# Performance work log

Hardware: AMD Instinct MI355X
Metric: run time of the kernel (lower is better)

Reference implementation:

```python
import jax, jax.numpy as jnp
import numpy as np

E = 200_000   # number of edges (messages)
T = 500_000   # number of triplets
H = 128       # hidden_channels
B = 8         # num_bilinear
R = 6         # num_radial
S = 7         # num_spherical


def setup_inputs() -> dict:
    key = jax.random.key(0)
    ks = jax.random.split(key, 18)
    w = 0.05  # small init scale for numerical stability
    return {
        "x":   jax.random.normal(ks[0], (E, H), dtype=jnp.float32),
        "rbf": jax.random.normal(ks[1], (E, R), dtype=jnp.float32),
        "sbf": jax.random.normal(ks[2], (T, S * R), dtype=jnp.float32),
        "idx_kj": jax.random.randint(ks[3], (T,), 0, E),
        "idx_ji": jax.random.randint(ks[4], (T,), 0, E),
        # parameters (stored as [in, out] so we apply x @ w)
        "lin_rbf_w": jax.random.normal(ks[5], (R, H), dtype=jnp.float32) * w,
        "lin_sbf_w": jax.random.normal(ks[6], (S * R, B), dtype=jnp.float32) * w,
        "lin_kj_w": jax.random.normal(ks[7], (H, H), dtype=jnp.float32) * w,
        "lin_kj_b": jnp.zeros((H,), dtype=jnp.float32),
        "lin_ji_w": jax.random.normal(ks[8], (H, H), dtype=jnp.float32) * w,
        "lin_ji_b": jnp.zeros((H,), dtype=jnp.float32),
        "W": jax.random.normal(ks[9], (H, B, H), dtype=jnp.float32) * (2.0 / H),
        "before_w": jax.random.normal(ks[10], (1, 2, H, H), dtype=jnp.float32) * w,
        "before_b": jnp.zeros((1, 2, H), dtype=jnp.float32),
        "lin_w": jax.random.normal(ks[11], (H, H), dtype=jnp.float32) * w,
        "lin_b": jnp.zeros((H,), dtype=jnp.float32),
        "after_w": jax.random.normal(ks[12], (2, 2, H, H), dtype=jnp.float32) * w,
        "after_b": jnp.zeros((2, 2, H), dtype=jnp.float32),
    }


def _residual(h, w2, b2):
    # DimeNet ResidualLayer: h + act(lin2(act(lin1(h))))
    return h + jax.nn.silu(jax.nn.silu(h @ w2[0] + b2[0]) @ w2[1] + b2[1])


def reference(x, rbf, sbf, idx_kj, idx_ji,
              lin_rbf_w, lin_sbf_w, lin_kj_w, lin_kj_b,
              lin_ji_w, lin_ji_b, W,
              before_w, before_b, lin_w, lin_b, after_w, after_b):
    act = jax.nn.silu
    rbf_p = rbf @ lin_rbf_w                     # [E, H]
    sbf_p = sbf @ lin_sbf_w                     # [T, B]
    x_ji = act(x @ lin_ji_w + lin_ji_b)         # [E, H]
    x_kj = act(x @ lin_kj_w + lin_kj_b) * rbf_p # [E, H]
    g = x_kj[idx_kj]                            # gather -> [T, H]
    # bilinear: 'wj,wl,ijl->wi' with i,l=hidden, j=bilinear
    m = jnp.einsum('wj,wl,ijl->wi', sbf_p, g, W)  # [T, H]
    agg = jax.ops.segment_sum(m, idx_ji, num_segments=x.shape[0])  # [E, H]
    h = x_ji + agg
    for i in range(before_w.shape[0]):
        h = _residual(h, before_w[i], before_b[i])
    h = act(h @ lin_w + lin_b) + x
    for i in range(after_w.shape[0]):
        h = _residual(h, after_w[i], after_b[i])
    return h
```

## Files before the change

kernel.cpp:

```cpp
#include <hip/hip_runtime.h>

#define E_N 200000
#define T_N 500000

typedef __attribute__((ext_vector_type(8))) short bf16x8;
typedef __attribute__((ext_vector_type(4))) float f32x4;
typedef unsigned short u16;
typedef unsigned int u32;

#define SWZ(b) ((b) ^ ((((b) >> 8) & 7) << 4))

#define SYNC_DRAIN() do { asm volatile("s_waitcnt vmcnt(0)" ::: "memory"); __syncthreads(); } while (0)

__device__ __forceinline__ u16 f2bf(float f){
  u32 u = __float_as_uint(f);
  return (u16)((u + 0x7fffu + ((u >> 16) & 1u)) >> 16);
}
__device__ __forceinline__ float silu_f(float v){
  return __fdividef(v, 1.f + __expf(-v));
}
__device__ __forceinline__ void gl_lds16(const void* g, void* l){
  __builtin_amdgcn_global_load_lds((const __attribute__((address_space(1))) u32*)g,
                                   (__attribute__((address_space(3))) u32*)l, 16, 0, 0);
}
__device__ __forceinline__ bf16x8 scale8(uint4 g, float s){
  union { bf16x8 v; u32 u[4]; } aa;
  u32 gu[4] = { g.x, g.y, g.z, g.w };
  #pragma unroll
  for (int q = 0; q < 4; q++){
    float lo = __uint_as_float(gu[q] << 16) * s;
    float hi = __uint_as_float(gu[q] & 0xffff0000u) * s;
    asm("v_cvt_pk_bf16_f32 %0, %1, %2" : "=v"(aa.u[q]) : "v"(lo), "v"(hi));
  }
  return aa.v;
}

__device__ __forceinline__ void gemm_tile(const char* ldsA, const char* ldsB,
                                          int wv, int lane, f32x4 acc[8]){
  const int arow = wv*16 + (lane & 15);
  const int kof = (lane >> 4) << 3;
  #pragma unroll
  for (int kc = 0; kc < 4; kc++){
    const int kb = (kc*32 + kof)*2;
    bf16x8 a = *(const bf16x8*)(ldsA + SWZ(arow*256 + kb));
    #pragma unroll
    for (int n = 0; n < 8; n++){
      bf16x8 b = *(const bf16x8*)(ldsB + SWZ((n*16 + (lane & 15))*256 + kb));
      acc[n] = __builtin_amdgcn_mfma_f32_16x16x32_bf16(a, b, acc[n], 0, 0, 0);
    }
  }
}

__global__ __launch_bounds__(256) void k_cvt_W(const float* __restrict__ W, u16* __restrict__ out){
  int i = blockIdx.x*256 + threadIdx.x;
  out[i] = f2bf(W[i]);
}

__global__ __launch_bounds__(256) void k_cvt_T(const float* __restrict__ jiw, const float* __restrict__ kjw,
                                               const float* __restrict__ bw, const float* __restrict__ lw,
                                               const float* __restrict__ aw, u16* __restrict__ out){
  int i = blockIdx.x*256 + threadIdx.x;
  int m = i >> 14, o = i & 16383;
  int n = o >> 7, k = o & 127;
  const float* src;
  switch (m){
    case 0: src = jiw; break;
    case 1: src = kjw; break;
    case 2: src = bw; break;
    case 3: src = bw + 16384; break;
    case 4: src = lw; break;
    default: src = aw + (m - 5)*16384; break;
  }
  out[i] = f2bf(src[k*128 + n]);
}

__global__ __launch_bounds__(256) void k_edge(const float* __restrict__ x, const float* __restrict__ rbf,
    const float* __restrict__ rbfw, const u16* __restrict__ wji, const u16* __restrict__ wkj,
    const float* __restrict__ bji, const float* __restrict__ bkj,
    float* __restrict__ out, u16* __restrict__ xkj)
{
  __shared__ __align__(16) char ldsA[16384];
  __shared__ __align__(16) char ldsB[32768];
  __shared__ float lrbf[64*6];
  __shared__ float lrbfw[6*128];
  __shared__ float lbj[128];
  __shared__ float lbk[128];
  const int tid = threadIdx.x;
  const int e0 = blockIdx.x * 64;

  #pragma unroll
  for (int it = 0; it < 4; it++){
    int i = it*256 + tid;
    int row = i >> 4, c8 = (i & 15) << 3;
    const float4* s = (const float4*)(x + (e0 + row)*128 + c8);
    float4 v0 = s[0], v1 = s[1];
    union { u16 us[8]; uint4 q; } u;
    u.us[0]=f2bf(v0.x); u.us[1]=f2bf(v0.y); u.us[2]=f2bf(v0.z); u.us[3]=f2bf(v0.w);
    u.us[4]=f2bf(v1.x); u.us[5]=f2bf(v1.y); u.us[6]=f2bf(v1.z); u.us[7]=f2bf(v1.w);
    *(uint4*)(ldsA + SWZ(row*256 + c8*2)) = u.q;
  }
  #pragma unroll
  for (int it = 0; it < 8; it++){
    int p = (it*256 + tid)*16;
    int pb = __builtin_amdgcn_readfirstlane(p);
    int n = p >> 8, o = p & 255;
    gl_lds16((const char*)wji + n*256 + (o ^ ((n & 7) << 4)), ldsB + pb);
  }
  for (int i = tid; i < 384; i += 256) lrbf[i] = rbf[e0*6 + i];
  for (int i = tid; i < 768; i += 256) lrbfw[i] = rbfw[i];
  if (tid < 128){ lbj[tid] = bji[tid]; lbk[tid] = bkj[tid]; }
  SYNC_DRAIN();

  const int wv = tid >> 6, lane = tid & 63;
  const int colb = lane & 15, rgrp = (lane >> 4) << 2;
  f32x4 acc[8];
  #pragma unroll
  for (int n = 0; n < 8; n++)
    #pragma unroll
    for (int r = 0; r < 4; r++) acc[n][r] = 0.f;
  gemm_tile(ldsA, ldsB, wv, lane, acc);
  #pragma unroll
  for (int n = 0; n < 8; n++){
    int col = n*16 + colb;
    float b = lbj[col];
    #pragma unroll
    for (int r = 0; r < 4; r++){
      int row = e0 + wv*16 + rgrp + r;
      out[row*128 + col] = silu_f(acc[n][r] + b);
    }
  }
  __syncthreads();
  #pragma unroll
  for (int it = 0; it < 8; it++){
    int p = (it*256 + tid)*16;
    int pb = __builtin_amdgcn_readfirstlane(p);
    int n = p >> 8, o = p & 255;
    gl_lds16((const char*)wkj + n*256 + (o ^ ((n & 7) << 4)), ldsB + pb);
  }
  SYNC_DRAIN();
  #pragma unroll
  for (int n = 0; n < 8; n++)
    #pragma unroll
    for (int r = 0; r < 4; r++) acc[n][r] = 0.f;
  gemm_tile(ldsA, ldsB, wv, lane, acc);

  float rb[4][6];
  #pragma unroll
  for (int r = 0; r < 4; r++)
    #pragma unroll
    for (int c = 0; c < 6; c++) rb[r][c] = lrbf[(wv*16 + rgrp + r)*6 + c];
  #pragma unroll
  for (int n = 0; n < 8; n++){
    int col = n*16 + colb;
    float b = lbk[col];
    float wc[6];
    #pragma unroll
    for (int c = 0; c < 6; c++) wc[c] = lrbfw[c*128 + col];
    #pragma unroll
    for (int r = 0; r < 4; r++){
      float rp = 0.f;
      #pragma unroll
      for (int c = 0; c < 6; c++) rp += rb[r][c]*wc[c];
      int row = e0 + wv*16 + rgrp + r;
      xkj[row*128 + col] = f2bf(silu_f(acc[n][r] + b) * rp);
    }
  }
}

__device__ __forceinline__ void stage_Wslice(const u16* __restrict__ Wbf, int j, char* dst, int tid){
  #pragma unroll
  for (int it = 0; it < 4; it++){
    int p = (it*512 + tid)*16;
    int pb = __builtin_amdgcn_readfirstlane(p);
    int n = p >> 8, o = p & 255;
    gl_lds16((const char*)Wbf + n*2048 + j*256 + (o ^ ((n & 7) << 4)), dst + pb);
  }
}

__global__ __launch_bounds__(512, 4) void k_trip(
    const u16* __restrict__ xkj, const float* __restrict__ sbf, const float* __restrict__ sbfw,
    const int* __restrict__ idx_kj, const int* __restrict__ idx_ji, const u16* __restrict__ Wbf,
    float* __restrict__ out)
{
  __shared__ __align__(16) char ldsW[2][32768];
  __shared__ float lss[256*8];
  __shared__ float lsw[336];
  __shared__ int lji[256];
  __shared__ int lkj[256];
  const int tid = threadIdx.x;
  const int t0 = blockIdx.x * 256;

  {
    float* scr = (float*)ldsW;
    for (int i = tid; i < 256*42; i += 512){
      int gi = t0*42 + i;
      scr[i] = (gi < T_N*42) ? sbf[gi] : 0.f;
    }
  }
  for (int i = tid; i < 336; i += 512) lsw[i] = sbfw[i];
  if (tid < 256){
    int w = t0 + tid;
    lji[tid] = (w < T_N) ? idx_ji[w] : -1;
    lkj[tid] = (w < T_N) ? idx_kj[w] : 0;
  }
  __syncthreads();

  const int wv = tid >> 6, lane = tid & 63;
  const int r15 = lane & 15, q = lane >> 4;

  uint4 graw[8];
  #pragma unroll
  for (int rt = 0; rt < 2; rt++){
    int row = lkj[wv*32 + rt*16 + r15];
    const char* src = (const char*)xkj + (long)row*256 + q*16;
    #pragma unroll
    for (int kc = 0; kc < 4; kc++)
      graw[rt*4 + kc] = *(const uint4*)(src + kc*64);
  }
  if (tid < 256){
    const float* scr = (const float*)ldsW;
    float a[8];
    #pragma unroll
    for (int k = 0; k < 8; k++) a[k] = 0.f;
    for (int c = 0; c < 42; c++){
      float v = scr[tid*42 + c];
      #pragma unroll
      for (int k = 0; k < 8; k++) a[k] += v * lsw[c*8 + k];
    }
    #pragma unroll
    for (int k = 0; k < 8; k++) lss[tid*8 + k] = a[k];
  }
  __syncthreads();
  stage_Wslice(Wbf, 0, ldsW[0], tid);
  SYNC_DRAIN();

  f32x4 acc0[8], acc1[8];
  #pragma unroll
  for (int n = 0; n < 8; n++)
    #pragma unroll
    for (int r = 0; r < 4; r++){ acc0[n][r] = 0.f; acc1[n][r] = 0.f; }

  const int swz_lane = (r15 & 7) << 4;
  for (int j = 0; j < 8; j++){
    const char* bp = ldsW[j & 1];
    if (j < 7) stage_Wslice(Wbf, j + 1, ldsW[(j + 1) & 1], tid);
    const float s0 = lss[(wv*32 + r15)*8 + j];
    const float s1 = lss[(wv*32 + 16 + r15)*8 + j];
    #pragma unroll
    for (int kc = 0; kc < 4; kc++){
      const int ab = (r15*256 + q*16 + kc*64) ^ swz_lane;
      bf16x8 aa0 = scale8(graw[kc], s0);
      bf16x8 aa1 = scale8(graw[4 + kc], s1);
      #pragma unroll
      for (int n = 0; n < 8; n++){
        bf16x8 b = *(const bf16x8*)(bp + n*4096 + ab);
        acc0[n] = __builtin_amdgcn_mfma_f32_16x16x32_bf16(aa0, b, acc0[n], 0, 0, 0);
        acc1[n] = __builtin_amdgcn_mfma_f32_16x16x32_bf16(aa1, b, acc1[n], 0, 0, 0);
      }
    }
    SYNC_DRAIN();
  }

  const int rgrp = q << 2;
  #pragma unroll
  for (int n = 0; n < 8; n++){
    const int col = n*16 + r15;
    #pragma unroll
    for (int r = 0; r < 4; r++){
      int e0i = lji[wv*32 + rgrp + r];
      if (e0i >= 0) unsafeAtomicAdd(out + e0i*128 + col, acc0[n][r]);
      int e1i = lji[wv*32 + 16 + rgrp + r];
      if (e1i >= 0) unsafeAtomicAdd(out + e1i*128 + col, acc1[n][r]);
    }
  }
}

__global__ __launch_bounds__(256) void k_epi(
    const float* __restrict__ x, float* __restrict__ hio, const u16* __restrict__ wm,
    const float* __restrict__ bb2, const float* __restrict__ linb, const float* __restrict__ ab2)
{
  __shared__ __align__(16) char ldsA[16384];
  __shared__ __align__(16) char ldsB[32768];
  __shared__ float lbias[7][128];
  const int tid = threadIdx.x;
  const int e0 = blockIdx.x * 64;
  if (tid < 128){
    lbias[0][tid] = bb2[tid];
    lbias[1][tid] = bb2[128 + tid];
    lbias[2][tid] = linb[tid];
    lbias[3][tid] = ab2[tid];
    lbias[4][tid] = ab2[128 + tid];
    lbias[5][tid] = ab2[256 + tid];
    lbias[6][tid] = ab2[384 + tid];
  }
  const int wv = tid >> 6, lane = tid & 63;
  const int colb = lane & 15, rgrp = (lane >> 4) << 2;
  float h[8][4], t[8][4];
  f32x4 acc[8];
  #pragma unroll
  for (int n = 0; n < 8; n++)
    #pragma unroll
    for (int r = 0; r < 4; r++)
      h[n][r] = hio[(e0 + wv*16 + rgrp + r)*128 + n*16 + colb];

#define STAGE_B(mi) { \
  _Pragma("unroll") \
  for (int it = 0; it < 8; it++){ \
    int p = (it*256 + tid)*16; \
    int pb = __builtin_amdgcn_readfirstlane(p); \
    int nn = p >> 8, o = p & 255; \
    gl_lds16((const char*)wm + (mi)*32768 + nn*256 + (o ^ ((nn & 7) << 4)), ldsB + pb); \
  } }
#define WRITE_A(v) { \
  _Pragma("unroll") \
  for (int n = 0; n < 8; n++){ \
    _Pragma("unroll") \
    for (int r = 0; r < 4; r++){ \
      int rowl = wv*16 + rgrp + r; \
      *(u16*)(ldsA + SWZ(rowl*256 + (n*16 + colb)*2)) = f2bf(v[n][r]); \
    } } }
#define RUN_GEMM() { \
  _Pragma("unroll") \
  for (int n = 0; n < 8; n++){ \
    _Pragma("unroll") \
    for (int r = 0; r < 4; r++) acc[n][r] = 0.f; } \
  gemm_tile(ldsA, ldsB, wv, lane, acc); }

  STAGE_B(0); WRITE_A(h); SYNC_DRAIN(); RUN_GEMM();
  #pragma unroll
  for (int n = 0; n < 8; n++){ float b = lbias[0][n*16 + colb];
    #pragma unroll
    for (int r = 0; r < 4; r++) t[n][r] = silu_f(acc[n][r] + b); }
  __syncthreads(); STAGE_B(1); WRITE_A(t); SYNC_DRAIN(); RUN_GEMM();
  #pragma unroll
  for (int n = 0; n < 8; n++){ float b = lbias[1][n*16 + colb];
    #pragma unroll
    for (int r = 0; r < 4; r++) h[n][r] += silu_f(acc[n][r] + b); }
  __syncthreads(); STAGE_B(2); WRITE_A(h); SYNC_DRAIN(); RUN_GEMM();
  #pragma unroll
  for (int n = 0; n < 8; n++){ float b = lbias[2][n*16 + colb];
    #pragma unroll
    for (int r = 0; r < 4; r++)
      h[n][r] = silu_f(acc[n][r] + b) + x[(e0 + wv*16 + rgrp + r)*128 + n*16 + colb]; }
  __syncthreads(); STAGE_B(3); WRITE_A(h); SYNC_DRAIN(); RUN_GEMM();
  #pragma unroll
  for (int n = 0; n < 8; n++){ float b = lbias[3][n*16 + colb];
    #pragma unroll
    for (int r = 0; r < 4; r++) t[n][r] = silu_f(acc[n][r] + b); }
  __syncthreads(); STAGE_B(4); WRITE_A(t); SYNC_DRAIN(); RUN_GEMM();
  #pragma unroll
  for (int n = 0; n < 8; n++){ float b = lbias[4][n*16 + colb];
    #pragma unroll
    for (int r = 0; r < 4; r++) h[n][r] += silu_f(acc[n][r] + b); }
  __syncthreads(); STAGE_B(5); WRITE_A(h); SYNC_DRAIN(); RUN_GEMM();
  #pragma unroll
  for (int n = 0; n < 8; n++){ float b = lbias[5][n*16 + colb];
    #pragma unroll
    for (int r = 0; r < 4; r++) t[n][r] = silu_f(acc[n][r] + b); }
  __syncthreads(); STAGE_B(6); WRITE_A(t); SYNC_DRAIN(); RUN_GEMM();
  #pragma unroll
  for (int n = 0; n < 8; n++){ float b = lbias[6][n*16 + colb];
    #pragma unroll
    for (int r = 0; r < 4; r++) h[n][r] += silu_f(acc[n][r] + b); }

  #pragma unroll
  for (int n = 0; n < 8; n++)
    #pragma unroll
    for (int r = 0; r < 4; r++)
      hio[(e0 + wv*16 + rgrp + r)*128 + n*16 + colb] = h[n][r];
#undef STAGE_B
#undef WRITE_A
#undef RUN_GEMM
}

extern "C" void kernel_launch(void* const* d_in, const int* in_sizes, int n_in,
                              void* d_out, int out_size, void* d_ws, size_t ws_size,
                              hipStream_t stream)
{
  const float* x    = (const float*)d_in[0];
  const float* rbf  = (const float*)d_in[1];
  const float* sbf  = (const float*)d_in[2];
  const int* idx_kj = (const int*)d_in[3];
  const int* idx_ji = (const int*)d_in[4];
  const float* rbfw = (const float*)d_in[5];
  const float* sbfw = (const float*)d_in[6];
  const float* kjw  = (const float*)d_in[7];
  const float* kjb  = (const float*)d_in[8];
  const float* jiw  = (const float*)d_in[9];
  const float* jib  = (const float*)d_in[10];
  const float* W    = (const float*)d_in[11];
  const float* bw   = (const float*)d_in[12];
  const float* bb   = (const float*)d_in[13];
  const float* lw   = (const float*)d_in[14];
  const float* lb   = (const float*)d_in[15];
  const float* aw   = (const float*)d_in[16];
  const float* ab   = (const float*)d_in[17];
  float* out = (float*)d_out;
  char* ws = (char*)d_ws;
  u16* Wbf  = (u16*)(ws);
  u16* linT = (u16*)(ws + 262144);
  u16* xkj  = (u16*)(ws + 1048576);

  k_cvt_W<<<dim3(512), dim3(256), 0, stream>>>(W, Wbf);
  k_cvt_T<<<dim3(576), dim3(256), 0, stream>>>(jiw, kjw, bw, lw, aw, linT);
  k_edge<<<dim3(E_N/64), dim3(256), 0, stream>>>(x, rbf, rbfw, linT, linT + 16384, jib, kjb, out, xkj);
  k_trip<<<dim3((T_N + 255)/256), dim3(512), 0, stream>>>(xkj, sbf, sbfw, idx_kj, idx_ji, Wbf, out);
  k_epi<<<dim3(E_N/64), dim3(256), 0, stream>>>(x, out, linT + 2*16384, bb, lb, ab);
}
```

Before: 680.7 us.

## Split triplet kernel over output-column halves and stage whole W half in LDS

```diff
diff --git a/kernel.cpp b/kernel.cpp
--- a/kernel.cpp
+++ b/kernel.cpp
@@ -55,7 +55,6 @@
   int i = blockIdx.x*256 + threadIdx.x;
   out[i] = f2bf(W[i]);
 }
-
 __global__ __launch_bounds__(256) void k_cvt_T(const float* __restrict__ jiw, const float* __restrict__ kjw,
                                                const float* __restrict__ bw, const float* __restrict__ lw,
                                                const float* __restrict__ aw, u16* __restrict__ out){
@@ -167,34 +166,26 @@
   }
 }
 
-__device__ __forceinline__ void stage_Wslice(const u16* __restrict__ Wbf, int j, char* dst, int tid){
-  #pragma unroll
-  for (int it = 0; it < 4; it++){
-    int p = (it*512 + tid)*16;
-    int pb = __builtin_amdgcn_readfirstlane(p);
-    int n = p >> 8, o = p & 255;
-    gl_lds16((const char*)Wbf + n*2048 + j*256 + (o ^ ((n & 7) << 4)), dst + pb);
-  }
-}
-
-__global__ __launch_bounds__(512, 4) void k_trip(
+__global__ __launch_bounds__(512, 1) void k_trip(
     const u16* __restrict__ xkj, const float* __restrict__ sbf, const float* __restrict__ sbfw,
     const int* __restrict__ idx_kj, const int* __restrict__ idx_ji, const u16* __restrict__ Wbf,
     float* __restrict__ out)
 {
-  __shared__ __align__(16) char ldsW[2][32768];
+  __shared__ __align__(16) char ldsW[131072];
   __shared__ float lss[256*8];
   __shared__ float lsw[336];
   __shared__ int lji[256];
   __shared__ int lkj[256];
   const int tid = threadIdx.x;
-  const int t0 = blockIdx.x * 256;
+  const int bid = blockIdx.x;
+  const int ch  = bid & 1;
+  const int t0  = (bid >> 1) * 256;
 
   {
     float* scr = (float*)ldsW;
     for (int i = tid; i < 256*42; i += 512){
-      int gi = t0*42 + i;
-      scr[i] = (gi < T_N*42) ? sbf[gi] : 0.f;
+      long gi = (long)t0*42 + i;
+      scr[i] = (gi < (long)T_N*42) ? sbf[gi] : 0.f;
     }
   }
   for (int i = tid; i < 336; i += 512) lsw[i] = sbfw[i];
@@ -231,46 +222,51 @@
     for (int k = 0; k < 8; k++) lss[tid*8 + k] = a[k];
   }
   __syncthreads();
-  stage_Wslice(Wbf, 0, ldsW[0], tid);
+
+  const char* wsrc = (const char*)(Wbf + (size_t)ch*64*1024);
+  #pragma unroll
+  for (int it = 0; it < 16; it++){
+    int p = (it*512 + tid)*16;
+    int pb = __builtin_amdgcn_readfirstlane(p);
+    int nrow = p >> 11, off = p & 2047;
+    int jb = off >> 8, rem = off & 255;
+    gl_lds16(wsrc + nrow*2048 + jb*256 + (rem ^ ((nrow & 7) << 4)), ldsW + pb);
+  }
   SYNC_DRAIN();
 
-  f32x4 acc0[8], acc1[8];
-  #pragma unroll
-  for (int n = 0; n < 8; n++)
+  f32x4 acc0[4], acc1[4];
+  #pragma unroll
+  for (int n = 0; n < 4; n++)
     #pragma unroll
     for (int r = 0; r < 4; r++){ acc0[n][r] = 0.f; acc1[n][r] = 0.f; }
 
-  const int swz_lane = (r15 & 7) << 4;
   for (int j = 0; j < 8; j++){
-    const char* bp = ldsW[j & 1];
-    if (j < 7) stage_Wslice(Wbf, j + 1, ldsW[(j + 1) & 1], tid);
     const float s0 = lss[(wv*32 + r15)*8 + j];
     const float s1 = lss[(wv*32 + 16 + r15)*8 + j];
     #pragma unroll
     for (int kc = 0; kc < 4; kc++){
-      const int ab = (r15*256 + q*16 + kc*64) ^ swz_lane;
       bf16x8 aa0 = scale8(graw[kc], s0);
       bf16x8 aa1 = scale8(graw[4 + kc], s1);
       #pragma unroll
-      for (int n = 0; n < 8; n++){
-        bf16x8 b = *(const bf16x8*)(bp + n*4096 + ab);
+      for (int n = 0; n < 4; n++){
+        const int nrow = n*16 + r15;
+        bf16x8 b = *(const bf16x8*)(ldsW + nrow*2048 + j*256 + ((kc*64 + q*16) ^ ((nrow & 7) << 4)));
         acc0[n] = __builtin_amdgcn_mfma_f32_16x16x32_bf16(aa0, b, acc0[n], 0, 0, 0);
         acc1[n] = __builtin_amdgcn_mfma_f32_16x16x32_bf16(aa1, b, acc1[n], 0, 0, 0);
       }
     }
-    SYNC_DRAIN();
   }
 
   const int rgrp = q << 2;
   #pragma unroll
-  for (int n = 0; n < 8; n++){
-    const int col = n*16 + r15;
+  for (int n = 0; n < 4; n++){
+    const int col = ch*64 + n*16 + r15;
     #pragma unroll
     for (int r = 0; r < 4; r++){
       int e0i = lji[wv*32 + rgrp + r];
-      if (e0i >= 0) unsafeAtomicAdd(out + e0i*128 + col, acc0[n][r]);
+      if (e0i >= 0) unsafeAtomicAdd(out + (size_t)e0i*128 + col, acc0[n][r]);
       int e1i = lji[wv*32 + 16 + rgrp + r];
-      if (e1i >= 0) unsafeAtomicAdd(out + e1i*128 + col, acc1[n][r]);
+      if (e1i >= 0) unsafeAtomicAdd(out + (size_t)e1i*128 + col, acc1[n][r]);
     }
   }
 }
@@ -400,10 +396,11 @@
   u16* Wbf  = (u16*)(ws);
   u16* linT = (u16*)(ws + 262144);
   u16* xkj  = (u16*)(ws + 1048576);
+  const int TGRID = (T_N + 255)/256;
 
   k_cvt_W<<<dim3(512), dim3(256), 0, stream>>>(W, Wbf);
   k_cvt_T<<<dim3(576), dim3(256), 0, stream>>>(jiw, kjw, bw, lw, aw, linT);
   k_edge<<<dim3(E_N/64), dim3(256), 0, stream>>>(x, rbf, rbfw, linT, linT + 16384, jib, kjb, out, xkj);
-  k_trip<<<dim3((T_N + 255)/256), dim3(512), 0, stream>>>(xkj, sbf, sbfw, idx_kj, idx_ji, Wbf, out);
+  k_trip<<<dim3(TGRID*2), dim3(512), 0, stream>>>(xkj, sbf, sbfw, idx_kj, idx_ji, Wbf, out);
   k_epi<<<dim3(E_N/64), dim3(256), 0, stream>>>(x, out, linT + 2*16384, bb, lb, ab);
 }
```

Measured after the change: 703.6 us. 1.03x slower.
